# Kernel tuning notes

Measured on AMD Instinct MI355X. Metric: run time of the kernel, lower is better.

The kernel has to match this reference:

```python
import jax, jax.numpy as jnp
import numpy as np

B, N, K, H, C = 16, 2048, 9, 128, 2  # K = nb_neighbors, kernel_size = K+1


def setup_inputs() -> dict:
    key = jax.random.key(0)
    ks = jax.random.split(key, 7)
    s = 0.1
    x = jax.random.normal(ks[0], (B, N, C), jnp.float32)
    Wconv = jax.random.normal(ks[1], (H, C, K + 1), jnp.float32) * s  # conv1d weight
    bconv = jax.random.normal(ks[2], (H,), jnp.float32) * s
    W1 = jax.random.normal(ks[3], (H, C), jnp.float32) * s
    b1 = jax.random.normal(ks[4], (H,), jnp.float32) * s
    W2 = jax.random.normal(ks[5], (H, H), jnp.float32) * s
    b2 = jax.random.normal(ks[6], (H,), jnp.float32) * s
    return {"x": x, "Wconv": Wconv, "bconv": bconv, "W1": W1, "b1": b1, "W2": W2, "b2": b2}


def reference(x, Wconv, bconv, W1, b1, W2, b2):
    # node embedding: W1(x)
    node_emb = jnp.einsum('bnc,hc->bnh', x, W1) + b1  # (B,N,H)

    # pairwise Euclidean distances (B,N,N) via the GEMM form
    sq = jnp.sum(x * x, axis=-1)  # (B,N)
    d2 = sq[:, :, None] + sq[:, None, :] - 2.0 * jnp.einsum('bnc,bmc->bnm', x, x)
    dist = jnp.sqrt(jnp.maximum(d2, 0.0))

    # torch: topk(k=N) (descending) then take last K+1 columns -> the K+1
    # smallest distances ordered descending (nearest/self last)
    knn = jnp.flip(jnp.argsort(dist, axis=-1)[..., : K + 1], axis=-1)  # (B,N,K+1)

    # batched gather of neighbor coords: (B,N,K+1,C)
    coords = jax.vmap(lambda xb, ib: xb[ib])(x, knn)

    # conv1d with kernel spanning the full window -> single output position,
    # i.e. a contraction over (channel, position)
    conv_emb = jnp.einsum('bnkc,hck->bnh', coords, Wconv) + bconv  # (B,N,H)
    conv_emb = jnp.einsum('bnh,eh->bne', conv_emb, W2) + b2

    return node_emb + conv_emb
```

## Files before the change

kernel.cpp:

```cpp
#include <hip/hip_runtime.h>
#include <cfloat>
#include <stdint.h>

#define B_   16
#define N_   2048
#define KK   10
#define H_   128
#define SUB  32
#define NCH  (N_ / SUB)

__device__ inline uint32_t f32_ordered(float f) {
    uint32_t u = __float_as_uint(f);
    return (u & 0x80000000u) ? ~u : (u | 0x80000000u);
}

__global__ __launch_bounds__(1024) void setup_kernel(
    const float* __restrict__ x,
    const float* __restrict__ Wconv, const float* __restrict__ bconv,
    const float* __restrict__ b1,    const float* __restrict__ W2,
    const float* __restrict__ b2,
    float4* __restrict__ xsorted,
    float*  __restrict__ weff,
    float*  __restrict__ btot)
{
#pragma clang fp contract(off)
    __shared__ uint64_t sk[N_];
    const int tid = threadIdx.x;
    if (blockIdx.x >= 16) {
        int gid = (blockIdx.x - 16) * 1024 + tid;
        if (gid < H_ * KK * 2) {
            int e = gid / 20, r = gid % 20, k = r >> 1, c = r & 1;
            float acc = 0.f;
            for (int h = 0; h < H_; ++h)
                acc += W2[e * H_ + h] * Wconv[h * (2 * KK) + c * KK + k];
            weff[gid] = acc;
        } else if (gid < H_ * KK * 2 + H_) {
            int e = gid - H_ * KK * 2;
            float acc = b1[e] + b2[e];
            for (int h = 0; h < H_; ++h) acc += W2[e * H_ + h] * bconv[h];
            btot[e] = acc;
        }
        return;
    }
    const int b = blockIdx.x;
    const float2* xb = (const float2*)(x + (size_t)b * N_ * 2);
    for (int i = tid; i < N_; i += 1024)
        sk[i] = ((uint64_t)f32_ordered(xb[i].x) << 32) | (uint32_t)i;
    __syncthreads();
    for (int size = 2; size <= N_; size <<= 1) {
        for (int stride = size >> 1; stride > 0; stride >>= 1) {
            int i = 2 * tid - (tid & (stride - 1));
            int j = i + stride;
            bool up = ((i & size) == 0);
            uint64_t a = sk[i], c = sk[j];
            if (up ? (a > c) : (a < c)) { sk[i] = c; sk[j] = a; }
            __syncthreads();
        }
    }
    for (int i = tid; i < N_; i += 1024) {
        uint32_t idx = (uint32_t)sk[i];
        float2 p = xb[idx];
        float sm = p.x * p.x + p.y * p.y;
        xsorted[(size_t)b * N_ + i] = make_float4(p.x, p.y, sm, __uint_as_float(idx));
    }
}

__global__ __launch_bounds__(512, 4) void knn_conv_kernel(
    const float4* __restrict__ xsorted,
    const float* __restrict__ W1,
    const float* __restrict__ weff,
    const float* __restrict__ btot,
    float* __restrict__ out)
{
#pragma clang fp contract(off)
    __shared__ float4   xs4[N_];
    __shared__ uint64_t mkeys[64 * 81];
    __shared__ float    wcoord[64 * 21];

    const int tid  = threadIdx.x;
    const int w    = tid >> 6;
    const int l    = tid & 63;
    const int b    = blockIdx.x >> 5;
    const int tile = blockIdx.x & 31;

    const float4* xb = xsorted + (size_t)b * N_;
    for (int i = tid; i < N_; i += 512) xs4[i] = xb[i];
    __syncthreads();

    const int    n  = tile * 64 + l;
    const float4 qv = xs4[n];
    const float  qx = qv.x, qy = qv.y, sqn = qv.z;
    const float  qa  = xs4[tile * 64].x;
    const float  qbx = xs4[tile * 64 + 63].x;

    const uint64_t KINIT = (((uint64_t)0x7F7FFFFFu) << 32) | 0x3FFFFFu;
    uint64_t hk[KK];
#pragma unroll
    for (int j = 0; j < KK; ++j) hk[j] = KINIT;
    float h9d = FLT_MAX;

    auto scan_chunk = [&](int mc) {
        for (int mm = 0; mm < SUB; ++mm) {
            const int m = mc + mm;
            float4 c4 = xs4[m];
            float s  = sqn + c4.z;
            float pr = qx * c4.x;
            float dt = __builtin_fmaf(qy, c4.y, pr);
            float d2 = __builtin_fmaf(-2.0f, dt, s);
            float dc = d2 > 0.0f ? d2 : 0.0f;
            if (dc <= h9d) {
                uint32_t oi = __float_as_uint(c4.w);
                uint64_t key = ((uint64_t)__float_as_uint(dc) << 32)
                             | (oi << 11) | (uint32_t)m;
                if (key < hk[KK - 1]) {
#pragma unroll
                    for (int j = KK - 1; j >= 1; --j) {
                        bool cj  = key < hk[j];
                        bool cjm = key < hk[j - 1];
                        hk[j] = cj ? (cjm ? hk[j - 1] : key) : hk[j];
                    }
                    hk[0] = (key < hk[0]) ? key : hk[0];
                }
                h9d = __uint_as_float((uint32_t)(hk[KK - 1] >> 32));
            }
        }
    };

    const int ct2 = 2 * tile;
    const int a   = (w - ct2) & 7;
    const int c1  = ct2 + a;
    const int c2  = c1 - 8;
    int c_near = (a <= 4) ? c1 : c2;
    if (c1 > NCH - 1) c_near = c2;
    if (c2 < 0)       c_near = c1;
    scan_chunk(c_near * SUB);

    int  cl = c_near - 8, cr = c_near + 8;
    bool la = (cl >= 0), ra = (cr <= NCH - 1);
    while (la || ra) {
        float wm = h9d;
        wm = fmaxf(wm, __shfl_xor(wm, 1,  64));
        wm = fmaxf(wm, __shfl_xor(wm, 2,  64));
        wm = fmaxf(wm, __shfl_xor(wm, 4,  64));
        wm = fmaxf(wm, __shfl_xor(wm, 8,  64));
        wm = fmaxf(wm, __shfl_xor(wm, 16, 64));
        wm = fmaxf(wm, __shfl_xor(wm, 32, 64));
        float gl = la ? (qa - xs4[cl * SUB + SUB - 1].x) : FLT_MAX;
        float gr = ra ? (xs4[cr * SUB].x - qbx)          : FLT_MAX;
        bool pickL = la && (!ra || gl <= gr);
        if (pickL) {
            if (__builtin_fmaf(gl, gl, -4e-6f) > wm) la = false;
            else { scan_chunk(cl * SUB); cl -= 8; la = (cl >= 0); }
        } else {
            if (__builtin_fmaf(gr, gr, -4e-6f) > wm) ra = false;
            else { scan_chunk(cr * SUB); cr += 8; ra = (cr <= NCH - 1); }
        }
    }

    {
        const int mb = l * 81 + w * 10;
#pragma unroll
        for (int j = 0; j < KK; ++j) mkeys[mb + j] = hk[j];
    }

    const int e = tid & 127;
    float we[20];
    {
        const float4* wp = (const float4*)(weff + e * 20);
#pragma unroll
        for (int r = 0; r < 5; ++r) {
            float4 v = wp[r];
            we[4 * r + 0] = v.x; we[4 * r + 1] = v.y;
            we[4 * r + 2] = v.z; we[4 * r + 3] = v.w;
        }
    }
    const float w1x = W1[e * 2 + 0];
    const float w1y = W1[e * 2 + 1];
    const float bt  = btot[e];
    __syncthreads();

    {
        const int q = tid >> 3;
        const int r = tid & 7;
        const int mb = q * 81 + r * 10;
        int p = 0;
#pragma unroll
        for (int sel = 0; sel < KK; ++sel) {
            uint64_t v = (p < KK) ? mkeys[mb + p] : 0xFFFFFFFFFFFFFFFFull;
            uint64_t t1 = __shfl_xor((unsigned long long)v, 1, 64);
            uint64_t m1 = v  < t1 ? v  : t1;
            uint64_t t2 = __shfl_xor((unsigned long long)m1, 2, 64);
            uint64_t m2 = m1 < t2 ? m1 : t2;
            uint64_t t4 = __shfl_xor((unsigned long long)m2, 4, 64);
            uint64_t vm = m2 < t4 ? m2 : t4;
            if (v == vm) {
                ++p;
                float4 c = xs4[(int)(vm & 0x7FF)];
                const int k = (KK - 1) - sel;
                wcoord[q * 21 + 2 * k + 0] = c.x;
                wcoord[q * 21 + 2 * k + 1] = c.y;
            }
        }
    }
    __syncthreads();

    const int qb_ = tid >> 7;
    const size_t obase = (size_t)b * N_ * H_;
#pragma unroll
    for (int jj = 0; jj < 16; ++jj) {
        const int qq = qb_ + 4 * jj;
        float4 xq = xs4[tile * 64 + qq];
        uint32_t orig = __float_as_uint(xq.w);
        const float* wc = &wcoord[qq * 21];
        float acc = bt;
        acc += xq.x * w1x;
        acc += xq.y * w1y;
#pragma unroll
        for (int k = 0; k < KK; ++k) {
            acc += wc[2 * k + 0] * we[2 * k + 0];
            acc += wc[2 * k + 1] * we[2 * k + 1];
        }
        out[obase + (size_t)orig * H_ + e] = acc;
    }
}

extern "C" void kernel_launch(void* const* d_in, const int* in_sizes, int n_in,
                              void* d_out, int out_size, void* d_ws, size_t ws_size,
                              hipStream_t stream) {
    const float* x     = (const float*)d_in[0];
    const float* Wconv = (const float*)d_in[1];
    const float* bconv = (const float*)d_in[2];
    const float* W1    = (const float*)d_in[3];
    const float* b1    = (const float*)d_in[4];
    const float* W2    = (const float*)d_in[5];
    const float* b2    = (const float*)d_in[6];
    float* out  = (float*)d_out;
    float* weff = (float*)d_ws;
    float* btot = weff + H_ * KK * 2;
    float4* xsorted = (float4*)((char*)d_ws + 16384);

    setup_kernel<<<dim3(19), dim3(1024), 0, stream>>>(
        x, Wconv, bconv, b1, W2, b2, xsorted, weff, btot);
    knn_conv_kernel<<<dim3(B_ * (N_ / 64)), dim3(512), 0, stream>>>(
        xsorted, W1, weff, btot, out);
}
```

Measured before the change: 163.0 us.

## Replace per-batch bitonic sort with parallel rank-counting sort across many small blocks

```diff
diff --git a/kernel.cpp b/kernel.cpp
--- a/kernel.cpp
+++ b/kernel.cpp
@@ -9,12 +9,16 @@
 #define SUB  32
 #define NCH  (N_ / SUB)
 
+#define RANK_BLOCKS (B_ * 16)
+#define WEFF_ELEMS  (H_ * KK * 2 + H_)
+#define WEFF_BLOCKS ((WEFF_ELEMS + 63) / 64)
+
 __device__ inline uint32_t f32_ordered(float f) {
     uint32_t u = __float_as_uint(f);
     return (u & 0x80000000u) ? ~u : (u | 0x80000000u);
 }
 
-__global__ __launch_bounds__(1024) void setup_kernel(
+__global__ __launch_bounds__(64) void setup_kernel(
     const float* __restrict__ x,
     const float* __restrict__ Wconv, const float* __restrict__ bconv,
     const float* __restrict__ b1,    const float* __restrict__ W2,
@@ -24,10 +28,11 @@
     float*  __restrict__ btot)
 {
 #pragma clang fp contract(off)
-    __shared__ uint64_t sk[N_];
+    __shared__ __align__(16) uint64_t sk[N_];
     const int tid = threadIdx.x;
-    if (blockIdx.x >= 16) {
-        int gid = (blockIdx.x - 16) * 1024 + tid;
+
+    if (blockIdx.x >= RANK_BLOCKS) {
+        int gid = (blockIdx.x - RANK_BLOCKS) * 64 + tid;
         if (gid < H_ * KK * 2) {
             int e = gid / 20, r = gid % 20, k = r >> 1, c = r & 1;
             float acc = 0.f;
@@ -42,27 +47,36 @@
         }
         return;
     }
-    const int b = blockIdx.x;
+
+    const int b   = blockIdx.x >> 4;
+    const int seg = blockIdx.x & 15;
     const float2* xb = (const float2*)(x + (size_t)b * N_ * 2);
-    for (int i = tid; i < N_; i += 1024)
+
+    for (int i = tid; i < N_; i += 64)
         sk[i] = ((uint64_t)f32_ordered(xb[i].x) << 32) | (uint32_t)i;
     __syncthreads();
-    for (int size = 2; size <= N_; size <<= 1) {
-        for (int stride = size >> 1; stride > 0; stride >>= 1) {
-            int i = 2 * tid - (tid & (stride - 1));
-            int j = i + stride;
-            bool up = ((i & size) == 0);
-            uint64_t a = sk[i], c = sk[j];
-            if (up ? (a > c) : (a < c)) { sk[i] = c; sk[j] = a; }
-            __syncthreads();
-        }
-    }
-    for (int i = tid; i < N_; i += 1024) {
-        uint32_t idx = (uint32_t)sk[i];
-        float2 p = xb[idx];
-        float sm = p.x * p.x + p.y * p.y;
-        xsorted[(size_t)b * N_ + i] = make_float4(p.x, p.y, sm, __uint_as_float(idx));
-    }
+
+    const int i0 = seg * 128 + tid;
+    const int i1 = i0 + 64;
+    const uint64_t k0 = sk[i0];
+    const uint64_t k1 = sk[i1];
+    int r0 = 0, r1 = 0;
+    const ulonglong2* sk2 = (const ulonglong2*)sk;
+#pragma unroll 8
+    for (int j = 0; j < N_ / 2; ++j) {
+        ulonglong2 kk = sk2[j];
+        r0 += (int)(kk.x < k0) + (int)(kk.y < k0);
+        r1 += (int)(kk.x < k1) + (int)(kk.y < k1);
+    }
+
+    float2 p0 = xb[i0];
+    float2 p1 = xb[i1];
+    float sm0 = p0.x * p0.x + p0.y * p0.y;
+    float sm1 = p1.x * p1.x + p1.y * p1.y;
+    xsorted[(size_t)b * N_ + r0] =
+        make_float4(p0.x, p0.y, sm0, __uint_as_float((uint32_t)i0));
+    xsorted[(size_t)b * N_ + r1] =
+        make_float4(p1.x, p1.y, sm1, __uint_as_float((uint32_t)i1));
 }
 
 __global__ __launch_bounds__(512, 4) void knn_conv_kernel(
@@ -239,7 +253,7 @@
     float* btot = weff + H_ * KK * 2;
     float4* xsorted = (float4*)((char*)d_ws + 16384);
 
-    setup_kernel<<<dim3(19), dim3(1024), 0, stream>>>(
+    setup_kernel<<<dim3(RANK_BLOCKS + WEFF_BLOCKS), dim3(64), 0, stream>>>(
         x, Wconv, bconv, b1, W2, b2, xsorted, weff, btot);
     knn_conv_kernel<<<dim3(B_ * (N_ / 64)), dim3(512), 0, stream>>>(
         xsorted, W1, weff, btot, out);
```

Result: slower. 180.7 us (+10.8%).
